# Kernel optimization log

Hardware: AMD Instinct MI355X
Metric: run time of the kernel (lower is better)

Reference implementation:

```python
import jax, jax.numpy as jnp
import numpy as np

V, E, H, CTX = 32000, 512, 1024, 1024
T, B = 64, 64

def setup_inputs() -> dict:
    key = jax.random.key(0)
    ks = jax.random.split(key, 16)
    s = lambda *sh: 1.0 / np.sqrt(sh[-1])
    inp = {
        "seq": jax.random.randint(ks[0], (T, B), 0, V, dtype=jnp.int32),
        "context": jax.random.normal(ks[1], (B, CTX), dtype=jnp.float32),
        "emb": jax.random.normal(ks[2], (V, E), dtype=jnp.float32) * 0.02,
        "W_ih": jax.random.normal(ks[3], (4 * H, E + CTX), dtype=jnp.float32) * s(E + CTX),
        "b_ih": jnp.zeros((4 * H,), dtype=jnp.float32),
        "W_hh": jax.random.normal(ks[4], (4 * H, H), dtype=jnp.float32) * s(H),
        "b_hh": jnp.zeros((4 * H,), dtype=jnp.float32),
        "W_initS": jax.random.normal(ks[5], (H, CTX), dtype=jnp.float32) * s(CTX),
        "b_initS": jnp.zeros((H,), dtype=jnp.float32),
        "W_initC": jax.random.normal(ks[6], (H, CTX), dtype=jnp.float32) * s(CTX),
        "b_initC": jnp.zeros((H,), dtype=jnp.float32),
        "W_d1": jax.random.normal(ks[7], (H, 2 * H), dtype=jnp.float32) * s(2 * H),
        "b_d1": jnp.zeros((H,), dtype=jnp.float32),
        "W_d2": jax.random.normal(ks[8], (V, H), dtype=jnp.float32) * s(H),
        "b_d2": jnp.zeros((V,), dtype=jnp.float32),
        "mode": 1,
    }
    return inp

def reference(seq, context, emb, W_ih, b_ih, W_hh, b_hh, W_initS, b_initS,
              W_initC, b_initC, W_d1, b_d1, W_d2, b_d2, mode):
    # init state from context (nonlinear = tanh); mode=1 -> eval path (no dropout)
    h0 = jnp.tanh(context @ W_initS.T + b_initS)  # [B,H]
    c0 = jnp.tanh(context @ W_initC.T + b_initC)  # [B,H]

    def step(carry, tok):
        h, c = carry
        x = jnp.concatenate([context, emb[tok]], axis=1)          # [B, CTX+E]
        gates = x @ W_ih.T + b_ih + h @ W_hh.T + b_hh             # [B, 4H]
        i_g, f_g, g_g, o_g = jnp.split(gates, 4, axis=1)
        c_new = jax.nn.sigmoid(f_g) * c + jax.nn.sigmoid(i_g) * jnp.tanh(g_g)
        h_new = jax.nn.sigmoid(o_g) * jnp.tanh(c_new)
        hid = jnp.tanh(jnp.concatenate([h_new, c_new], axis=1) @ W_d1.T + b_d1)  # [B,H]
        out = hid @ W_d2.T + b_d2                                  # [B,V]
        return (h_new, c_new), out

    _, outputs = jax.lax.scan(step, (h0, c0), seq)  # [T,B,V]
    return outputs
```

## Files before the change

### kernel.cpp

```cpp
#include <hip/hip_runtime.h>
#include <hip/hip_bf16.h>
#include <cstdint>

#define V_  32000
#define E_  512
#define H_  1024
#define CTX_ 1024
#define T_  64
#define B_  64
#define FH_ 4096
#define NRB 128

typedef __attribute__((ext_vector_type(8))) __bf16 bf16x8;
typedef __attribute__((ext_vector_type(4))) __bf16 bf16x4;
typedef __attribute__((ext_vector_type(4))) float f32x4;

#define DEV static __device__ __forceinline__

DEV __bf16 f2bf(float f) {
    union { float f; unsigned u; } v; v.f = f;
    unsigned r = (v.u + 0x7FFFu + ((v.u >> 16) & 1u)) >> 16;
    unsigned short s = (unsigned short)r;
    return __builtin_bit_cast(__bf16, s);
}

DEV float sigm(float x) { return 1.0f / (1.0f + __expf(-x)); }

DEV unsigned long long ld8cc(const __bf16* p) {
    return __hip_atomic_load((const unsigned long long*)p,
                             __ATOMIC_RELAXED, __HIP_MEMORY_SCOPE_AGENT);
}
DEV void st8cc(__bf16* p, unsigned long long v) {
    __hip_atomic_store((unsigned long long*)p, v,
                       __ATOMIC_RELAXED, __HIP_MEMORY_SCOPE_AGENT);
}

#define GL(g, l) __builtin_amdgcn_global_load_lds(                         \
    (const __attribute__((address_space(1))) void*)(g),                    \
    (__attribute__((address_space(3))) void*)(l), 16, 0, 0)

__global__ __launch_bounds__(256) void k_cast(const float* __restrict__ src,
                                              __bf16* __restrict__ dst, int n4) {
    int i = blockIdx.x * 256 + threadIdx.x;
    if (i >= n4) return;
    float4 v = *(const float4*)(src + (size_t)i * 4);
    bf16x4 o; o[0]=f2bf(v.x); o[1]=f2bf(v.y); o[2]=f2bf(v.z); o[3]=f2bf(v.w);
    *(bf16x4*)(dst + (size_t)i * 4) = o;
}

__global__ __launch_bounds__(256) void k_cast_wihe(const float* __restrict__ Wih,
                                                   __bf16* __restrict__ dst) {
    int i = blockIdx.x * 256 + threadIdx.x;
    int e = i * 4, j = e >> 9, k = e & 511;
    float4 v = *(const float4*)(Wih + (size_t)j * (CTX_ + E_) + CTX_ + k);
    bf16x4 o; o[0]=f2bf(v.x); o[1]=f2bf(v.y); o[2]=f2bf(v.z); o[3]=f2bf(v.w);
    *(bf16x4*)(dst + (size_t)e) = o;
}

__global__ __launch_bounds__(256) void k_gather_x(const int* __restrict__ seq,
                                                  const float* __restrict__ emb,
                                                  __bf16* __restrict__ dst) {
    int i = blockIdx.x * 256 + threadIdx.x;
    int e = i * 4, r = e >> 9, k = e & 511;
    int tok = seq[r];
    float4 v = *(const float4*)(emb + (size_t)tok * E_ + k);
    bf16x4 o; o[0]=f2bf(v.x); o[1]=f2bf(v.y); o[2]=f2bf(v.z); o[3]=f2bf(v.w);
    *(bf16x4*)(dst + (size_t)e) = o;
}

__global__ __launch_bounds__(256) void k_init(const float* __restrict__ ctx,
                                              const float* __restrict__ WS, const float* __restrict__ bS,
                                              const float* __restrict__ WC, const float* __restrict__ bC,
                                              __bf16* __restrict__ h0, float* __restrict__ c0) {
    int idx = blockIdx.x * 256 + threadIdx.x;
    int r = idx >> 4, bg = idx & 15;
    int sel = r >> 10, u = r & 1023;
    const float4* w = (const float4*)((sel ? WC : WS) + (size_t)u * CTX_);
    float acc[4] = {0.f,0.f,0.f,0.f};
    for (int k = 0; k < 256; ++k) {
        float4 wv = w[k];
#pragma unroll
        for (int i = 0; i < 4; ++i) {
            float4 cv = *(const float4*)(ctx + (size_t)(bg + 16*i) * CTX_ + k * 4);
            acc[i] += wv.x*cv.x + wv.y*cv.y + wv.z*cv.z + wv.w*cv.w;
        }
    }
    float bias = sel ? bC[u] : bS[u];
#pragma unroll
    for (int i = 0; i < 4; ++i) {
        int b = bg + 16*i;
        float v = tanhf(acc[i] + bias);
        if (sel) c0[(size_t)b * H_ + u] = v;
        else     h0[(size_t)b * 2048 + u] = f2bf(v);
    }
}

__global__ __launch_bounds__(256) void k_ctxgates(const float* __restrict__ ctx,
                                                  const float* __restrict__ Wih,
                                                  const float* __restrict__ bih,
                                                  const float* __restrict__ bhh,
                                                  float* __restrict__ out) {
    int idx = blockIdx.x * 256 + threadIdx.x;
    int j = idx >> 4, bg = idx & 15;
    const float4* w = (const float4*)(Wih + (size_t)j * (CTX_ + E_));
    float acc[4] = {0.f,0.f,0.f,0.f};
    for (int k = 0; k < 256; ++k) {
        float4 wv = w[k];
#pragma unroll
        for (int i = 0; i < 4; ++i) {
            float4 cv = *(const float4*)(ctx + (size_t)(bg + 16*i) * CTX_ + k * 4);
            acc[i] += wv.x*cv.x + wv.y*cv.y + wv.z*cv.z + wv.w*cv.w;
        }
    }
    float bias = bih[j] + bhh[j];
#pragma unroll
    for (int i = 0; i < 4; ++i) out[(size_t)(bg + 16*i) * FH_ + j] = acc[i] + bias;
}

__global__ __launch_bounds__(1024) void k_zero(unsigned* __restrict__ bar) {
    bar[threadIdx.x] = 0u;
}

__global__ __launch_bounds__(512, 2) void k_rnn(
    const __bf16* __restrict__ Whh, const __bf16* __restrict__ WihE,
    const __bf16* __restrict__ Xb, const float* __restrict__ ctxg,
    const float* __restrict__ c0,
    __bf16* __restrict__ HCx, unsigned* __restrict__ bar)
{
    __shared__ float red[8][64][36];
    __shared__ __bf16 hnb[64][8];
    __shared__ __bf16 cnb[64][8];
    const int tid = threadIdx.x;
    const int w = tid >> 6, lane = tid & 63;
    const int fr = lane & 15, fq = lane >> 4;
    const int u0 = (int)blockIdx.x * 8;
    const int kb = w * 192;

    bf16x8 breg[2][6];
#pragma unroll
    for (int ni = 0; ni < 2; ++ni) {
        const int n = ni * 16 + fr;
        const int j = (n >> 3) * H_ + u0 + (n & 7);
#pragma unroll
        for (int ks = 0; ks < 6; ++ks) {
            const int k = kb + ks * 32;
            const __bf16* src = (k < H_) ? (Whh + (size_t)j * H_ + k)
                                         : (WihE + (size_t)j * E_ + (k - H_));
            breg[ni][ks] = *(const bf16x8*)(src + fq * 8);
        }
    }
    const int cb = tid >> 3, cul = tid & 7, u = u0 + cul;
    float creg = c0[(size_t)cb * H_ + u];
    float cg[4];
#pragma unroll
    for (int g = 0; g < 4; ++g) cg[g] = ctxg[(size_t)cb * FH_ + g * H_ + u];

#pragma unroll 1
    for (int t = 0; t < T_; ++t) {
        const __bf16* hprev = HCx + (size_t)t * (B_ * 2 * H_);
        __bf16*       hcur  = HCx + (size_t)(t + 1) * (B_ * 2 * H_);
        const __bf16* Xt = Xb + (size_t)t * (B_ * E_);

        f32x4 acc[4][2];
#pragma unroll
        for (int mi = 0; mi < 4; ++mi)
#pragma unroll
            for (int ni = 0; ni < 2; ++ni) acc[mi][ni] = (f32x4){0.f,0.f,0.f,0.f};

#pragma unroll
        for (int ks = 0; ks < 6; ++ks) {
            const int k = kb + ks * 32;
            bf16x8 af[4];
            if (k < H_) {
#pragma unroll
                for (int mi = 0; mi < 4; ++mi) {
                    const __bf16* s = hprev + (size_t)(mi * 16 + fr) * 2048 + k + fq * 8;
                    union { unsigned long long q[2]; bf16x8 v; } uu;
                    uu.q[0] = ld8cc(s); uu.q[1] = ld8cc(s + 4);
                    af[mi] = uu.v;
                }
            } else {
#pragma unroll
                for (int mi = 0; mi < 4; ++mi)
                    af[mi] = *(const bf16x8*)(Xt + (size_t)(mi * 16 + fr) * E_ + (k - H_) + fq * 8);
            }
#pragma unroll
            for (int mi = 0; mi < 4; ++mi)
#pragma unroll
                for (int ni = 0; ni < 2; ++ni)
                    acc[mi][ni] = __builtin_amdgcn_mfma_f32_16x16x32_bf16(
                        af[mi], breg[ni][ks], acc[mi][ni], 0, 0, 0);
        }
#pragma unroll
        for (int mi = 0; mi < 4; ++mi)
#pragma unroll
            for (int ni = 0; ni < 2; ++ni)
#pragma unroll
                for (int r = 0; r < 4; ++r)
                    red[w][mi * 16 + fq * 4 + r][ni * 16 + fr] = acc[mi][ni][r];
        __syncthreads();

        float gv[4];
#pragma unroll
        for (int g = 0; g < 4; ++g) {
            float s = cg[g];
#pragma unroll
            for (int wv = 0; wv < 8; ++wv) s += red[wv][cb][g * 8 + cul];
            gv[g] = s;
        }
        const float cn = sigm(gv[1]) * creg + sigm(gv[0]) * tanhf(gv[2]);
        const float hn = sigm(gv[3]) * tanhf(cn);
        creg = cn;
        hnb[cb][cul] = f2bf(hn);
        cnb[cb][cul] = f2bf(cn);
        __syncthreads();

        if (tid < 256) {
            const int b = tid >> 2, sel = (tid >> 1) & 1, hf = tid & 1;
            const __bf16* s = sel ? &cnb[b][hf * 4] : &hnb[b][hf * 4];
            unsigned long long q = *(const unsigned long long*)s;
            st8cc(hcur + (size_t)b * 2048 + sel * H_ + u0 + hf * 4, q);
        }

        __syncthreads();
        if (tid == 0) {
            unsigned* b4 = bar + t * 16;
            __hip_atomic_fetch_add(b4, 1u, __ATOMIC_RELAXED, __HIP_MEMORY_SCOPE_AGENT);
            while (__hip_atomic_load(b4, __ATOMIC_RELAXED, __HIP_MEMORY_SCOPE_AGENT)
                   < (unsigned)NRB) { }
        }
        __syncthreads();
    }
}

__global__ __launch_bounds__(256) void k_gemm_d1(const __bf16* __restrict__ A,
                                                 const __bf16* __restrict__ Bt,
                                                 const float* __restrict__ bias,
                                                 __bf16* __restrict__ C,
                                                 int M, int N, int K) {
    __shared__ __align__(16) char smem[16384];
    __bf16* Als = (__bf16*)smem;
    __bf16* Bls = (__bf16*)(smem + 8192);
    const int tid = threadIdx.x, lane = tid & 63, wave = tid >> 6;
    const int wm = wave >> 1, wn = wave & 1;
    const int bm = blockIdx.y * 128, bn = blockIdx.x * 128;
    const int srow = wave * 16 + (lane >> 2);
    const int scol = (lane & 3) * 8;
    const int fr = lane & 15, fq = lane >> 4;

    f32x4 acc[4][4];
#pragma unroll
    for (int i = 0; i < 4; ++i)
#pragma unroll
        for (int j = 0; j < 4; ++j) acc[i][j] = (f32x4){0.f,0.f,0.f,0.f};

    const int nkt = K >> 5;
    for (int kt = 0; kt < nkt; ++kt) {
        const int k0 = kt << 5;
        GL(A  + (size_t)(bm + srow) * K + k0 + scol,      smem + wave * 1024);
        GL(A  + (size_t)(bm + 64 + srow) * K + k0 + scol, smem + 4096 + wave * 1024);
        GL(Bt + (size_t)(bn + srow) * K + k0 + scol,      smem + 8192 + wave * 1024);
        GL(Bt + (size_t)(bn + 64 + srow) * K + k0 + scol, smem + 12288 + wave * 1024);
        __syncthreads();
        bf16x8 af[4], bfr[4];
#pragma unroll
        for (int mi = 0; mi < 4; ++mi)
            af[mi] = *(const bf16x8*)(Als + (wm*64 + mi*16 + fr) * 32 + fq * 8);
#pragma unroll
        for (int ni = 0; ni < 4; ++ni)
            bfr[ni] = *(const bf16x8*)(Bls + (wn*64 + ni*16 + fr) * 32 + fq * 8);
#pragma unroll
        for (int mi = 0; mi < 4; ++mi)
#pragma unroll
            for (int ni = 0; ni < 4; ++ni)
                acc[mi][ni] = __builtin_amdgcn_mfma_f32_16x16x32_bf16(af[mi], bfr[ni], acc[mi][ni], 0, 0, 0);
        __syncthreads();
    }
    const int cr = fq * 4, cc = fr;
#pragma unroll
    for (int ni = 0; ni < 4; ++ni) {
        const int gc = bn + wn*64 + ni*16 + cc;
        const float bv = bias[gc];
#pragma unroll
        for (int mi = 0; mi < 4; ++mi) {
            const int gr = bm + wm*64 + mi*16 + cr;
#pragma unroll
            for (int r = 0; r < 4; ++r)
                C[(size_t)(gr + r) * N + gc] = f2bf(tanhf(acc[mi][ni][r] + bv));
        }
    }
}

__global__ __launch_bounds__(256) void k_gemm_bt(const __bf16* __restrict__ A,
                                                 const __bf16* __restrict__ Bt,
                                                 const float* __restrict__ bias,
                                                 float* __restrict__ C,
                                                 int M, int N, int K) {
    __shared__ __align__(16) char smem[16384];
    __bf16* Als = (__bf16*)smem;
    __bf16* Bls = (__bf16*)(smem + 8192);
    const int tid = threadIdx.x, lane = tid & 63, wave = tid >> 6;
    const int wm = wave >> 1, wn = wave & 1;
    const int bm = blockIdx.y * 128, bn = blockIdx.x * 128;
    const int srow = wave * 16 + (lane >> 2);
    const int scol = (lane & 3) * 8;
    const int fr = lane & 15, fq = lane >> 4;

    f32x4 acc[4][4];
#pragma unroll
    for (int i = 0; i < 4; ++i)
#pragma unroll
        for (int j = 0; j < 4; ++j) acc[i][j] = (f32x4){0.f,0.f,0.f,0.f};

    const int nkt = K >> 5;
    for (int kt = 0; kt < nkt; ++kt) {
        const int k0 = kt << 5;
        GL(A  + (size_t)(bm + srow) * K + k0 + scol,      smem + wave * 1024);
        GL(A  + (size_t)(bm + 64 + srow) * K + k0 + scol, smem + 4096 + wave * 1024);
        GL(Bt + (size_t)(bn + srow) * K + k0 + scol,      smem + 8192 + wave * 1024);
        GL(Bt + (size_t)(bn + 64 + srow) * K + k0 + scol, smem + 12288 + wave * 1024);
        __syncthreads();
        bf16x8 af[4], bfr[4];
#pragma unroll
        for (int mi = 0; mi < 4; ++mi)
            af[mi] = *(const bf16x8*)(Als + (wm*64 + mi*16 + fr) * 32 + fq * 8);
#pragma unroll
        for (int ni = 0; ni < 4; ++ni)
            bfr[ni] = *(const bf16x8*)(Bls + (wn*64 + ni*16 + fr) * 32 + fq * 8);
#pragma unroll
        for (int mi = 0; mi < 4; ++mi)
#pragma unroll
            for (int ni = 0; ni < 4; ++ni)
                acc[mi][ni] = __builtin_amdgcn_mfma_f32_16x16x32_bf16(af[mi], bfr[ni], acc[mi][ni], 0, 0, 0);
        __syncthreads();
    }
    const int cr = fq * 4, cc = fr;
#pragma unroll
    for (int ni = 0; ni < 4; ++ni) {
        const int gc = bn + wn*64 + ni*16 + cc;
        const float bv = bias ? bias[gc] : 0.f;
#pragma unroll
        for (int mi = 0; mi < 4; ++mi) {
            const int gr = bm + wm*64 + mi*16 + cr;
            float* cp = C + (size_t)gr * N + gc;
#pragma unroll
            for (int r = 0; r < 4; ++r) cp[(size_t)r * N] = acc[mi][ni][r] + bv;
        }
    }
}

extern "C" void kernel_launch(void* const* d_in, const int* in_sizes, int n_in,
                              void* d_out, int out_size, void* d_ws, size_t ws_size,
                              hipStream_t stream) {
    const int*   seq     = (const int*)d_in[0];
    const float* ctx     = (const float*)d_in[1];
    const float* emb     = (const float*)d_in[2];
    const float* W_ih    = (const float*)d_in[3];
    const float* b_ih    = (const float*)d_in[4];
    const float* W_hh    = (const float*)d_in[5];
    const float* b_hh    = (const float*)d_in[6];
    const float* W_initS = (const float*)d_in[7];
    const float* b_initS = (const float*)d_in[8];
    const float* W_initC = (const float*)d_in[9];
    const float* b_initC = (const float*)d_in[10];
    const float* W_d1    = (const float*)d_in[11];
    const float* b_d1    = (const float*)d_in[12];
    const float* W_d2    = (const float*)d_in[13];
    const float* b_d2    = (const float*)d_in[14];
    float* out = (float*)d_out;

    char* ws = (char*)d_ws;
    __bf16* Whh_bf  = (__bf16*)(ws + 0);
    __bf16* WihE_bf = (__bf16*)(ws + (8u << 20));
    __bf16* Wd1_bf  = (__bf16*)(ws + (12u << 20));
    __bf16* Wd2_bf  = (__bf16*)(ws + (16u << 20));
    __bf16* X_bf    = (__bf16*)(ws + 82313216u);
    float*  ctxg    = (float*) (ws + 86507520u);
    float*  cbuf    = (float*) (ws + 87556096u);
    __bf16* HCx     = (__bf16*)(ws + 87818240u);
    unsigned* bar   = (unsigned*)(ws + 104857600u);
    __bf16* hid     = (__bf16*)(ws + 0);

    k_cast<<<4096, 256, 0, stream>>>(W_hh, Whh_bf, 1048576);
    k_cast_wihe<<<2048, 256, 0, stream>>>(W_ih, WihE_bf);
    k_cast<<<2048, 256, 0, stream>>>(W_d1, Wd1_bf, 524288);
    k_cast<<<32000, 256, 0, stream>>>(W_d2, Wd2_bf, 8192000);
    k_gather_x<<<2048, 256, 0, stream>>>(seq, emb, X_bf);
    k_init<<<128, 256, 0, stream>>>(ctx, W_initS, b_initS, W_initC, b_initC, HCx, cbuf);
    k_ctxgates<<<256, 256, 0, stream>>>(ctx, W_ih, b_ih, b_hh, ctxg);
    k_zero<<<1, 1024, 0, stream>>>(bar);

    k_rnn<<<NRB, 512, 0, stream>>>(Whh_bf, WihE_bf, X_bf, ctxg, cbuf, HCx, bar);

    k_gemm_d1<<<dim3(H_ / 128, (T_ * B_) / 128), 256, 0, stream>>>(
        HCx + (size_t)B_ * 2 * H_, Wd1_bf, b_d1, hid, T_ * B_, H_, 2 * H_);

    k_gemm_bt<<<dim3(V_ / 128, (T_ * B_) / 128), 256, 0, stream>>>(
        hid, Wd2_bf, b_d2, out, T_ * B_, V_, H_);
}
```

Before: 2.165 ms.

## Use plain vector loads with acquire fence in RNN; XCD-aware GEMM tile mapping

The recurrent kernel now reads the previous hidden state with ordinary 16-byte vector loads, replacing paired relaxed atomic 8-byte loads, and adds an agent-scope acquire fence after the grid barrier spin so the loads still see the other blocks' stores. The two output GEMMs switch to a 1D grid with a remap that gives each XCD a contiguous band of M rows, so blocks sharing A tiles land on the same L2. The intent is wider loads on the serial recurrence critical path and better L2 reuse in the large vocab GEMM. It relies on the fence making non-atomic loads coherent across CUs, and the remap assumes the M tile count divides by 8.

```diff
diff --git a/kernel.cpp b/kernel.cpp
--- a/kernel.cpp
+++ b/kernel.cpp
@@ -26,10 +26,6 @@
 
 DEV float sigm(float x) { return 1.0f / (1.0f + __expf(-x)); }
 
-DEV unsigned long long ld8cc(const __bf16* p) {
-    return __hip_atomic_load((const unsigned long long*)p,
-                             __ATOMIC_RELAXED, __HIP_MEMORY_SCOPE_AGENT);
-}
 DEV void st8cc(__bf16* p, unsigned long long v) {
     __hip_atomic_store((unsigned long long*)p, v,
                        __ATOMIC_RELAXED, __HIP_MEMORY_SCOPE_AGENT);
@@ -171,18 +167,13 @@
         for (int ks = 0; ks < 6; ++ks) {
             const int k = kb + ks * 32;
             bf16x8 af[4];
-            if (k < H_) {
-#pragma unroll
-                for (int mi = 0; mi < 4; ++mi) {
-                    const __bf16* s = hprev + (size_t)(mi * 16 + fr) * 2048 + k + fq * 8;
-                    union { unsigned long long q[2]; bf16x8 v; } uu;
-                    uu.q[0] = ld8cc(s); uu.q[1] = ld8cc(s + 4);
-                    af[mi] = uu.v;
-                }
-            } else {
-#pragma unroll
-                for (int mi = 0; mi < 4; ++mi)
-                    af[mi] = *(const bf16x8*)(Xt + (size_t)(mi * 16 + fr) * E_ + (k - H_) + fq * 8);
+#pragma unroll
+            for (int mi = 0; mi < 4; ++mi) {
+                const int row = mi * 16 + fr;
+                const __bf16* src = (k < H_)
+                    ? (hprev + (size_t)row * 2048 + k + fq * 8)
+                    : (Xt + (size_t)row * E_ + (k - H_) + fq * 8);
+                af[mi] = *(const bf16x8*)src;
             }
 #pragma unroll
             for (int mi = 0; mi < 4; ++mi)
@@ -228,9 +219,17 @@
             __hip_atomic_fetch_add(b4, 1u, __ATOMIC_RELAXED, __HIP_MEMORY_SCOPE_AGENT);
             while (__hip_atomic_load(b4, __ATOMIC_RELAXED, __HIP_MEMORY_SCOPE_AGENT)
                    < (unsigned)NRB) { }
-        }
-        __syncthreads();
-    }
+            __builtin_amdgcn_fence(__ATOMIC_ACQUIRE, "agent");
+        }
+        __syncthreads();
+    }
+}
+
+DEV void xcd_tiles(int bid, int ntx, int nty, int& x, int& y) {
+    const int xcd = bid & 7, i = bid >> 3;
+    const int cy = nty >> 3;
+    x = i / cy;
+    y = xcd * cy + (i % cy);
 }
 
 __global__ __launch_bounds__(256) void k_gemm_d1(const __bf16* __restrict__ A,
@@ -243,7 +242,8 @@
     __bf16* Bls = (__bf16*)(smem + 8192);
     const int tid = threadIdx.x, lane = tid & 63, wave = tid >> 6;
     const int wm = wave >> 1, wn = wave & 1;
-    const int bm = blockIdx.y * 128, bn = blockIdx.x * 128;
+    int tx, ty; xcd_tiles(blockIdx.x, N >> 7, M >> 7, tx, ty);
+    const int bm = ty * 128, bn = tx * 128;
     const int srow = wave * 16 + (lane >> 2);
     const int scol = (lane & 3) * 8;
     const int fr = lane & 15, fq = lane >> 4;
@@ -301,7 +301,8 @@
     __bf16* Bls = (__bf16*)(smem + 8192);
     const int tid = threadIdx.x, lane = tid & 63, wave = tid >> 6;
     const int wm = wave >> 1, wn = wave & 1;
-    const int bm = blockIdx.y * 128, bn = blockIdx.x * 128;
+    int tx, ty; xcd_tiles(blockIdx.x, N >> 7, M >> 7, tx, ty);
+    const int bm = ty * 128, bn = tx * 128;
     const int srow = wave * 16 + (lane >> 2);
     const int scol = (lane & 3) * 8;
     const int fr = lane & 15, fq = lane >> 4;
@@ -392,9 +393,9 @@
 
     k_rnn<<<NRB, 512, 0, stream>>>(Whh_bf, WihE_bf, X_bf, ctxg, cbuf, HCx, bar);
 
-    k_gemm_d1<<<dim3(H_ / 128, (T_ * B_) / 128), 256, 0, stream>>>(
+    k_gemm_d1<<<(H_ / 128) * ((T_ * B_) / 128), 256, 0, stream>>>(
         HCx + (size_t)B_ * 2 * H_, Wd1_bf, b_d1, hid, T_ * B_, H_, 2 * H_);
 
-    k_gemm_bt<<<dim3(V_ / 128, (T_ * B_) / 128), 256, 0, stream>>>(
+    k_gemm_bt<<<(V_ / 128) * ((T_ * B_) / 128), 256, 0, stream>>>(
         hid, Wd2_bf, b_d2, out, T_ * B_, V_, H_);
 }
```

Result: faster. 2.013 ms (-7.0%).
